# Kernel optimization log

Measured on AMD Instinct MI355X. Metric: run time of the kernel, lower is better.

## Reference

```python
import jax, jax.numpy as jnp
import numpy as np

B, H, L, D = 4, 4096, 8, 64  # queries shape [B, L, H, D]
FACTOR = 5
U = FACTOR * int(np.ceil(np.log(4096)))  # u_part = u = 45 (L_q == L_k)


def setup_inputs() -> dict:
    key = jax.random.key(0)
    kq, kk, kv, ki = jax.random.split(key, 4)
    queries = jax.random.normal(kq, (4, 4096, 8, 64), dtype=jnp.float32)
    keys = jax.random.normal(kk, (4, 4096, 8, 64), dtype=jnp.float32)
    values = jax.random.normal(kv, (4, 4096, 8, 64), dtype=jnp.float32)
    index_sample = jax.random.randint(ki, (4096, U), 0, 4096)  # torch.randint(key_length,(L_Q,sample_k))
    return {"queries": queries, "keys": keys, "values": values, "index_sample": index_sample}


def reference(queries, keys, values, index_sample):
    # (B, L, H, D) -> (B, H, L, D)
    q = jnp.transpose(queries, (0, 2, 1, 3))
    k = jnp.transpose(keys, (0, 2, 1, 3))
    v = jnp.transpose(values, (0, 2, 1, 3))
    b, h, l_q, d = q.shape
    l_k = k.shape[2]
    n_top = index_sample.shape[1]  # u == u_part == 45 here

    # --- _prob_QK: sampled QK scores (avoid materializing key_expand [B,H,Lq,Lk,D]) ---
    # key_sample: [B, H, Lq, sample_k, D]
    key_sample = k[:, :, index_sample, :]
    # Q_i . K_sampled: [B, H, Lq, sample_k]
    qk_sample = jnp.einsum('bhld,bhlsd->bhls', q, key_sample)
    # sparsity measure M = max - mean(over full key_length)
    m = jnp.max(qk_sample, axis=-1) - jnp.sum(qk_sample, axis=-1) / l_k  # [B,H,Lq]
    _, m_top = jax.lax.top_k(m, n_top)  # [B, H, u]

    # reduced queries: [B, H, u, D]
    q_reduce = jnp.take_along_axis(q, m_top[..., None], axis=2)
    scores_top = jnp.einsum('bhud,bhkd->bhuk', q_reduce, k)  # [B, H, u, Lk]

    scale = 1.0 / jnp.sqrt(jnp.asarray(d, dtype=q.dtype))
    scores_top = scores_top * scale

    # --- _get_initial_context (mask_flag=False): mean of values broadcast over queries ---
    context = jnp.broadcast_to(jnp.mean(v, axis=2, keepdims=True), (b, h, l_q, d))

    # --- _update_context: softmax + scatter attn@V into the top-u query rows ---
    attn = jax.nn.softmax(scores_top, axis=-1)  # [B, H, u, Lk]
    update = jnp.einsum('bhuk,bhkd->bhud', attn, v)  # [B, H, u, D]
    b_idx = jnp.arange(b)[:, None, None]
    h_idx = jnp.arange(h)[None, :, None]
    context = context.at[b_idx, h_idx, m_top].set(update)
    return context  # [B, H, Lq, D]
```

## Files before the change

kernel.cpp:

```cpp
#include <hip/hip_runtime.h>
#include <hip/hip_bf16.h>


#define NB 4
#define NH 8
#define NL 4096
#define ND 64
#define NS 45
#define SCALE 0.125f
#define NCHUNK 16
#define CHUNK 256

typedef float floatx4 __attribute__((ext_vector_type(4)));

static __device__ __forceinline__ float neg_inf() { return -__builtin_inff(); }

template <int CTRL>
static __device__ __forceinline__ float dpp_add(float x) {
  int y = __builtin_amdgcn_update_dpp(0, __builtin_bit_cast(int, x), CTRL,
                                      0xF, 0xF, true);
  return x + __builtin_bit_cast(float, y);
}
static __device__ __forceinline__ float red16(float x) {
  x = dpp_add<0x140>(x);
  x = dpp_add<0x141>(x);
  x = dpp_add<0x4E>(x);
  x = dpp_add<0xB1>(x);
  return x;
}
static __device__ __forceinline__ float red4(float x) {
  x = dpp_add<0xB1>(x);
  x = dpp_add<0x4E>(x);
  return x;
}

__global__ __launch_bounds__(256) void k_compute_m(
    const float* __restrict__ q, const float* __restrict__ k,
    const int* __restrict__ idxs, float* __restrict__ m_out)
{
  __shared__ int sidx[4][48];
  int gb = blockIdx.x;
  int pair = gb & 7;
  int b = pair >> 1, hg = pair & 1;
  int lg = gb >> 3;
  int t = threadIdx.x, w = t >> 6, lane = t & 63, g = lane >> 4;
  int l = lg * 4 + w;

  if (lane < NS) sidx[w][lane] = idxs[l * NS + lane];

  const floatx4* q4 =
      (const floatx4*)(q + ((size_t)(b * NL + l) * NH + hg * 4) * ND);
  floatx4 qr = __builtin_nontemporal_load(q4 + lane);

  const float* kbase = k + ((size_t)b * NL * NH + hg * 4) * ND;

  float mx = neg_inf(), sm = 0.f;
#pragma unroll 1
  for (int s0 = 0; s0 < NS; s0 += 9) {
    floatx4 kr[9];
#pragma unroll
    for (int j = 0; j < 9; j++) {
      int ki = __builtin_amdgcn_readfirstlane(sidx[w][s0 + j]);
      kr[j] = *((const floatx4*)(kbase + (size_t)ki * 512) + lane);
    }
    float p[9];
#pragma unroll
    for (int j = 0; j < 9; j++) {
      float d = kr[j].x * qr.x + kr[j].y * qr.y + kr[j].z * qr.z + kr[j].w * qr.w;
      p[j] = red16(d);
    }
    float m0 = fmaxf(fmaxf(p[0], p[1]), p[2]);
    float m1 = fmaxf(fmaxf(p[3], p[4]), p[5]);
    float m2 = fmaxf(fmaxf(p[6], p[7]), p[8]);
    mx = fmaxf(fmaxf(mx, m0), fmaxf(m1, m2));
    sm += ((p[0] + p[1]) + (p[2] + p[3])) +
          ((p[4] + p[5]) + (p[6] + p[7])) + p[8];
  }
  if ((lane & 15) == 0)
    m_out[((size_t)b * NH + hg * 4 + g) * NL + l] = mx - sm * (1.0f / 4096.0f);
}

__global__ __launch_bounds__(256) void k_topk_p1(
    const float* __restrict__ m_in, unsigned long long* __restrict__ cand)
{
  __shared__ unsigned long long keys[512];
  __shared__ unsigned long long wred[4];
  int blk = blockIdx.x;
  int bh = blk >> 3, slice = blk & 7;
  int t = threadIdx.x, wid = t >> 6, lane = t & 63;
  int base = slice * 512;
  for (int i = t; i < 512; i += 256) {
    float v = m_in[bh * NL + base + i];
    unsigned u = __float_as_uint(v);
    u ^= (u >> 31) ? 0xFFFFFFFFu : 0x80000000u;
    keys[i] = ((unsigned long long)u << 32) | (unsigned)(~(unsigned)(base + i));
  }
  __syncthreads();
  for (int it = 0; it < NS; ++it) {
    unsigned long long k0 = keys[t], k1 = keys[t + 256];
    unsigned long long best = k0 > k1 ? k0 : k1;
#pragma unroll
    for (int off = 32; off; off >>= 1) {
      unsigned long long o = __shfl_xor(best, off);
      if (o > best) best = o;
    }
    if (lane == 0) wred[wid] = best;
    __syncthreads();
    if (t == 0) {
      unsigned long long b0 = wred[0];
      if (wred[1] > b0) b0 = wred[1];
      if (wred[2] > b0) b0 = wred[2];
      if (wred[3] > b0) b0 = wred[3];
      cand[blk * NS + it] = b0;
      int gi = (int)(~(unsigned)(b0 & 0xFFFFFFFFull));
      keys[gi - base] = 0;
    }
    __syncthreads();
  }
}

__global__ __launch_bounds__(256) void k_topk_p2(
    const unsigned long long* __restrict__ cand, int* __restrict__ mtop)
{
  __shared__ unsigned long long keys[8 * NS];
  __shared__ unsigned long long wred[4];
  __shared__ unsigned long long sbest;
  int bh = blockIdx.x;
  int t = threadIdx.x, wid = t >> 6, lane = t & 63;
  for (int i = t; i < 8 * NS; i += 256) keys[i] = cand[bh * 8 * NS + i];
  __syncthreads();
  for (int it = 0; it < NS; ++it) {
    unsigned long long best = (t < 8 * NS) ? keys[t] : 0ull;
    if (t + 256 < 8 * NS) {
      unsigned long long k1 = keys[t + 256];
      if (k1 > best) best = k1;
    }
#pragma unroll
    for (int off = 32; off; off >>= 1) {
      unsigned long long o = __shfl_xor(best, off);
      if (o > best) best = o;
    }
    if (lane == 0) wred[wid] = best;
    __syncthreads();
    if (t == 0) {
      unsigned long long b0 = wred[0];
      if (wred[1] > b0) b0 = wred[1];
      if (wred[2] > b0) b0 = wred[2];
      if (wred[3] > b0) b0 = wred[3];
      sbest = b0;
      mtop[bh * NS + it] = (int)(~(unsigned)(b0 & 0xFFFFFFFFull));
    }
    __syncthreads();
    unsigned long long bb = sbest;
    if (t < 8 * NS && keys[t] == bb) keys[t] = 0;
    if (t + 256 < 8 * NS && keys[t + 256] == bb) keys[t + 256] = 0;
    __syncthreads();
  }
}

__global__ __launch_bounds__(256) void k_meanv_part(
    const float* __restrict__ v, float* __restrict__ vpart)
{
  __shared__ float part[4][ND];
  int bh = blockIdx.x, c = blockIdx.y;
  int b = bh >> 3, h = bh & 7;
  int t = threadIdx.x, d = t & 63, g = t >> 6;
  float a0 = 0.f, a1 = 0.f, a2 = 0.f, a3 = 0.f;
  const float* vb = v + ((size_t)(b * NL + c * 64) * NH + h) * ND + d;
#pragma unroll
  for (int i = 0; i < 4; i++) {
    a0 += vb[(size_t)(g + 4 * (4 * i + 0)) * NH * ND];
    a1 += vb[(size_t)(g + 4 * (4 * i + 1)) * NH * ND];
    a2 += vb[(size_t)(g + 4 * (4 * i + 2)) * NH * ND];
    a3 += vb[(size_t)(g + 4 * (4 * i + 3)) * NH * ND];
  }
  part[g][d] = (a0 + a1) + (a2 + a3);
  __syncthreads();
  if (g == 0) {
    float s = part[0][d] + part[1][d] + part[2][d] + part[3][d];
    vpart[(bh * 64 + c) * ND + d] = s;
  }
}

__global__ __launch_bounds__(64) void k_meanv_final(
    const float* __restrict__ vpart, float* __restrict__ meanv)
{
  int bh = blockIdx.x, d = threadIdx.x;
  float s = 0.f;
  for (int c = 0; c < 64; c++) s += vpart[(bh * 64 + c) * ND + d];
  meanv[bh * ND + d] = s * (1.0f / 4096.0f);
}

__global__ __launch_bounds__(256) void k_fill(
    const float* __restrict__ meanv, float4* __restrict__ out4)
{
  const int total = NB * NH * NL * ND / 4;
  const float4* mv4 = (const float4*)meanv;
  for (int i = blockIdx.x * 256 + threadIdx.x; i < total; i += gridDim.x * 256) {
    int bh = i >> 16;
    int d4 = i & 15;
    out4[i] = mv4[bh * 16 + d4];
  }
}

__global__ __launch_bounds__(1024) void k_scores(
    const float* __restrict__ q, const float* __restrict__ k,
    const float* __restrict__ v, const int* __restrict__ mtop,
    float* __restrict__ mc_out, float* __restrict__ lc_out,
    float* __restrict__ op_out)
{
  __shared__ float QLDS[NS * ND];
  __shared__ float SLDS[NS * 260];
  __shared__ int mt[NS];
  __shared__ float mcs[NS], lcs[NS];

  int gb = blockIdx.x;
  int xcd = gb & 7, seq = gb >> 3;
  int bh = xcd * 4 + (seq >> 4);
  int c = seq & 15;
  int b = bh >> 3, h = bh & 7;
  int t = threadIdx.x;
  int wid = t >> 6, lane = t & 63;

  if (t < NS) mt[t] = mtop[bh * NS + t];
  __syncthreads();

  const float4* q4 = (const float4*)q;
  float4* QL4 = (float4*)QLDS;
  if (t < NS * 16) {
    int u = t >> 4, j = t & 15;
    QL4[t] = q4[((size_t)(b * NL + mt[u]) * NH + h) * 16 + j];
  }
  __syncthreads();

  {
    int kk = wid * 16 + (lane >> 2);
    int seg = lane & 3;
    const float4* k4 =
        (const float4*)(k + ((size_t)(b * NL + c * CHUNK + kk) * NH + h) * ND)
        + seg * 4;
    float4 k0 = k4[0], k1 = k4[1], k2 = k4[2], k3 = k4[3];
    const float4* qp = QL4 + seg * 4;
    for (int u = 0; u < NS; ++u) {
      float4 a0 = qp[u * 16 + 0], a1 = qp[u * 16 + 1];
      float4 a2 = qp[u * 16 + 2], a3 = qp[u * 16 + 3];
      float dot = a0.x * k0.x + a0.y * k0.y + a0.z * k0.z + a0.w * k0.w
                + a1.x * k1.x + a1.y * k1.y + a1.z * k1.z + a1.w * k1.w
                + a2.x * k2.x + a2.y * k2.y + a2.z * k2.z + a2.w * k2.w
                + a3.x * k3.x + a3.y * k3.y + a3.z * k3.z + a3.w * k3.w;
      dot = red4(dot);
      if (seg == 0) SLDS[u * 260 + kk] = dot * SCALE;
    }
  }
  __syncthreads();

  for (int u = wid; u < NS; u += 16) {
    float4 sv = *(const float4*)&SLDS[u * 260 + lane * 4];
    float mx = fmaxf(fmaxf(sv.x, sv.y), fmaxf(sv.z, sv.w));
#pragma unroll
    for (int off = 32; off; off >>= 1) mx = fmaxf(mx, __shfl_xor(mx, off));
    float e0 = expf(sv.x - mx), e1 = expf(sv.y - mx);
    float e2 = expf(sv.z - mx), e3 = expf(sv.w - mx);
    float s = e0 + e1 + e2 + e3;
#pragma unroll
    for (int off = 32; off; off >>= 1) s += __shfl_xor(s, off);
    *(float4*)&SLDS[u * 260 + lane * 4] = make_float4(e0, e1, e2, e3);
    if (lane == 0) { mcs[u] = mx; lcs[u] = s; }
  }
  __syncthreads();

  float acc[3];
#pragma unroll
  for (int i = 0; i < 3; i++) acc[i] = 0.f;
  const float* vbase = v + ((size_t)(b * NL + c * CHUNK) * NH + h) * ND + lane;
  for (int kb = 0; kb < 64; ++kb) {
    float vd0 = vbase[(size_t)(kb * 4 + 0) * NH * ND];
    float vd1 = vbase[(size_t)(kb * 4 + 1) * NH * ND];
    float vd2 = vbase[(size_t)(kb * 4 + 2) * NH * ND];
    float vd3 = vbase[(size_t)(kb * 4 + 3) * NH * ND];
#pragma unroll
    for (int i = 0; i < 3; i++) {
      int u = wid + 16 * i;
      if (u < NS) {
        float4 p4 = *(const float4*)&SLDS[u * 260 + kb * 4];
        acc[i] += p4.x * vd0 + p4.y * vd1 + p4.z * vd2 + p4.w * vd3;
      }
    }
  }
#pragma unroll
  for (int i = 0; i < 3; i++) {
    int u = wid + 16 * i;
    if (u < NS)
      op_out[(((size_t)bh * NCHUNK + c) * NS + u) * ND + lane] = acc[i];
  }
  if (t < NS) {
    mc_out[(bh * NCHUNK + c) * NS + t] = mcs[t];
    lc_out[(bh * NCHUNK + c) * NS + t] = lcs[t];
  }
}

__global__ __launch_bounds__(256) void k_combine(
    const float* __restrict__ mc, const float* __restrict__ lc,
    const float* __restrict__ op, const int* __restrict__ mtop,
    float* __restrict__ out)
{
  int gw = blockIdx.x * 4 + (threadIdx.x >> 6);
  int lane = threadIdx.x & 63;
  int bh = gw / NS, u = gw % NS;
  float M = neg_inf();
  for (int c = 0; c < NCHUNK; c++)
    M = fmaxf(M, mc[(bh * NCHUNK + c) * NS + u]);
  float Lsum = 0.f, O = 0.f;
  for (int c = 0; c < NCHUNK; c++) {
    float e = expf(mc[(bh * NCHUNK + c) * NS + u] - M);
    Lsum += lc[(bh * NCHUNK + c) * NS + u] * e;
    O += op[(((size_t)bh * NCHUNK + c) * NS + u) * ND + lane] * e;
  }
  int row = mtop[bh * NS + u];
  out[((size_t)bh * NL + row) * ND + lane] = O / Lsum;
}

extern "C" void kernel_launch(void* const* d_in, const int* in_sizes, int n_in,
                              void* d_out, int out_size, void* d_ws, size_t ws_size,
                              hipStream_t stream) {
  const float* q = (const float*)d_in[0];
  const float* k = (const float*)d_in[1];
  const float* v = (const float*)d_in[2];
  const int* idxs = (const int*)d_in[3];
  float* out = (float*)d_out;
  float* ws = (float*)d_ws;

  float* m_ws  = ws;
  int*   mtop  = (int*)(ws + 131072);
  float* meanv = ws + 132512;
  float* mc    = ws + 134560;
  float* lc    = ws + 157600;
  float* op    = ws + 180640;
  float* vpart = op;
  unsigned long long* cand = (unsigned long long*)(op + 131072);

  hipLaunchKernelGGL(k_compute_m,   dim3(8192),      dim3(256),  0, stream, q, k, idxs, m_ws);
  hipLaunchKernelGGL(k_topk_p1,     dim3(256),       dim3(256),  0, stream, m_ws, cand);
  hipLaunchKernelGGL(k_topk_p2,     dim3(32),        dim3(256),  0, stream, cand, mtop);
  hipLaunchKernelGGL(k_meanv_part,  dim3(32, 64),    dim3(256),  0, stream, v, vpart);
  hipLaunchKernelGGL(k_meanv_final, dim3(32),        dim3(64),   0, stream, vpart, meanv);
  hipLaunchKernelGGL(k_fill,        dim3(2048),      dim3(256),  0, stream, meanv, (float4*)out);
  hipLaunchKernelGGL(k_scores,      dim3(512),       dim3(1024), 0, stream, q, k, v, mtop, mc, lc, op);
  hipLaunchKernelGGL(k_combine,     dim3(360),       dim3(256),  0, stream, mc, lc, op, mtop, out);
}
```

Before: 186.3 us.

## Fuse meanv, topk2 and fill into neighbouring kernels to cut launches

Merges the V partial-mean reduction into the sampled-QK kernel as extra blocks, and the final mean into the second top-k pass as extra blocks. The output fill becomes extra blocks of the scores kernel. The QK sampling now splits the 45 samples across two waves per query, with an LDS combine. The goal is to cut launch gaps and overlap independent memory-bound work, at the cost of heterogeneous blocks and a 1024-thread fill that may compete with scores for CUs.

```diff
diff --git a/kernel.cpp b/kernel.cpp
--- a/kernel.cpp
+++ b/kernel.cpp
@@ -34,50 +34,93 @@
   return x;
 }
 
-__global__ __launch_bounds__(256) void k_compute_m(
+template <int BS>
+static __device__ __forceinline__ void batch_dot(
+    const float* __restrict__ kbase, const int* __restrict__ srow, int s0,
+    floatx4 qr, int lane, float& mx, float& sm) {
+  floatx4 kr[BS];
+#pragma unroll
+  for (int j = 0; j < BS; j++) {
+    int ki = __builtin_amdgcn_readfirstlane(srow[s0 + j]);
+    kr[j] = *((const floatx4*)(kbase + (size_t)ki * 512) + lane);
+  }
+  float p[BS];
+#pragma unroll
+  for (int j = 0; j < BS; j++) {
+    float d = kr[j].x * qr.x + kr[j].y * qr.y + kr[j].z * qr.z + kr[j].w * qr.w;
+    p[j] = red16(d);
+  }
+#pragma unroll
+  for (int j = 0; j < BS; j++) { mx = fmaxf(mx, p[j]); sm += p[j]; }
+}
+
+__global__ __launch_bounds__(512) void kA_m_meanv(
     const float* __restrict__ q, const float* __restrict__ k,
-    const int* __restrict__ idxs, float* __restrict__ m_out)
+    const float* __restrict__ v, const int* __restrict__ idxs,
+    float* __restrict__ m_out, float* __restrict__ vpart)
 {
   __shared__ int sidx[4][48];
+  __shared__ float lmx[8][4], lsm[8][4];
+  __shared__ float part[8][ND];
   int gb = blockIdx.x;
-  int pair = gb & 7;
-  int b = pair >> 1, hg = pair & 1;
-  int lg = gb >> 3;
   int t = threadIdx.x, w = t >> 6, lane = t & 63, g = lane >> 4;
-  int l = lg * 4 + w;
-
-  if (lane < NS) sidx[w][lane] = idxs[l * NS + lane];
-
-  const floatx4* q4 =
-      (const floatx4*)(q + ((size_t)(b * NL + l) * NH + hg * 4) * ND);
-  floatx4 qr = __builtin_nontemporal_load(q4 + lane);
-
-  const float* kbase = k + ((size_t)b * NL * NH + hg * 4) * ND;
-
-  float mx = neg_inf(), sm = 0.f;
-#pragma unroll 1
-  for (int s0 = 0; s0 < NS; s0 += 9) {
-    floatx4 kr[9];
-#pragma unroll
-    for (int j = 0; j < 9; j++) {
-      int ki = __builtin_amdgcn_readfirstlane(sidx[w][s0 + j]);
-      kr[j] = *((const floatx4*)(kbase + (size_t)ki * 512) + lane);
-    }
-    float p[9];
-#pragma unroll
-    for (int j = 0; j < 9; j++) {
-      float d = kr[j].x * qr.x + kr[j].y * qr.y + kr[j].z * qr.z + kr[j].w * qr.w;
-      p[j] = red16(d);
-    }
-    float m0 = fmaxf(fmaxf(p[0], p[1]), p[2]);
-    float m1 = fmaxf(fmaxf(p[3], p[4]), p[5]);
-    float m2 = fmaxf(fmaxf(p[6], p[7]), p[8]);
-    mx = fmaxf(fmaxf(mx, m0), fmaxf(m1, m2));
-    sm += ((p[0] + p[1]) + (p[2] + p[3])) +
-          ((p[4] + p[5]) + (p[6] + p[7])) + p[8];
-  }
-  if ((lane & 15) == 0)
-    m_out[((size_t)b * NH + hg * 4 + g) * NL + l] = mx - sm * (1.0f / 4096.0f);
+
+  if (gb < 8192) {
+    int pair = gb & 7;
+    int b = pair >> 1, hg = pair & 1;
+    int lg = gb >> 3;
+    int wl = w & 3;
+    int l = lg * 4 + wl;
+
+    if (w < 4 && lane < NS) sidx[w][lane] = idxs[l * NS + lane];
+
+    const floatx4* q4 =
+        (const floatx4*)(q + ((size_t)(b * NL + l) * NH + hg * 4) * ND);
+    floatx4 qr = __builtin_nontemporal_load(q4 + lane);
+    const float* kbase = k + ((size_t)b * NL * NH + hg * 4) * ND;
+    const int* srow = sidx[wl];
+    __syncthreads();
+
+    float mx = neg_inf(), sm = 0.f;
+    if (w < 4) {
+      batch_dot<8>(kbase, srow, 0, qr, lane, mx, sm);
+      batch_dot<8>(kbase, srow, 8, qr, lane, mx, sm);
+      batch_dot<8>(kbase, srow, 16, qr, lane, mx, sm);
+    } else {
+      batch_dot<7>(kbase, srow, 24, qr, lane, mx, sm);
+      batch_dot<7>(kbase, srow, 31, qr, lane, mx, sm);
+      batch_dot<7>(kbase, srow, 38, qr, lane, mx, sm);
+    }
+    if ((lane & 15) == 0) { lmx[w][g] = mx; lsm[w][g] = sm; }
+    __syncthreads();
+    if (w < 4 && (lane & 15) == 0) {
+      float MX = fmaxf(lmx[w][g], lmx[w + 4][g]);
+      float SM = lsm[w][g] + lsm[w + 4][g];
+      m_out[((size_t)b * NH + hg * 4 + g) * NL + l] = MX - SM * (1.0f / 4096.0f);
+    }
+  } else {
+    int idx = gb - 8192;
+    int bh = idx >> 5, cc = idx & 31;
+    int b = bh >> 3, h = bh & 7;
+    int d = t & 63, gg = t >> 6;
+    float a0 = 0.f, a1 = 0.f, a2 = 0.f, a3 = 0.f;
+    const float* vb = v + ((size_t)(b * NL + cc * 128) * NH + h) * ND + d;
+#pragma unroll
+    for (int i = 0; i < 4; i++) {
+      a0 += vb[(size_t)(gg + 8 * (4 * i + 0)) * NH * ND];
+      a1 += vb[(size_t)(gg + 8 * (4 * i + 1)) * NH * ND];
+      a2 += vb[(size_t)(gg + 8 * (4 * i + 2)) * NH * ND];
+      a3 += vb[(size_t)(gg + 8 * (4 * i + 3)) * NH * ND];
+    }
+    part[gg][d] = (a0 + a1) + (a2 + a3);
+    __syncthreads();
+    if (gg == 0) {
+      float s = 0.f;
+#pragma unroll
+      for (int j = 0; j < 8; j++) s += part[j][d];
+      vpart[(bh * 32 + cc) * ND + d] = s;
+    }
+  }
 }
 
 __global__ __launch_bounds__(256) void k_topk_p1(
@@ -119,95 +162,69 @@
   }
 }
 
-__global__ __launch_bounds__(256) void k_topk_p2(
-    const unsigned long long* __restrict__ cand, int* __restrict__ mtop)
+__global__ __launch_bounds__(256) void kC_topk2_meanv(
+    const unsigned long long* __restrict__ cand, int* __restrict__ mtop,
+    const float* __restrict__ vpart, float* __restrict__ meanv)
 {
   __shared__ unsigned long long keys[8 * NS];
   __shared__ unsigned long long wred[4];
   __shared__ unsigned long long sbest;
-  int bh = blockIdx.x;
+  __shared__ float part2[4][ND];
+  int gb = blockIdx.x;
   int t = threadIdx.x, wid = t >> 6, lane = t & 63;
-  for (int i = t; i < 8 * NS; i += 256) keys[i] = cand[bh * 8 * NS + i];
-  __syncthreads();
-  for (int it = 0; it < NS; ++it) {
-    unsigned long long best = (t < 8 * NS) ? keys[t] : 0ull;
-    if (t + 256 < 8 * NS) {
-      unsigned long long k1 = keys[t + 256];
-      if (k1 > best) best = k1;
-    }
-#pragma unroll
-    for (int off = 32; off; off >>= 1) {
-      unsigned long long o = __shfl_xor(best, off);
-      if (o > best) best = o;
-    }
-    if (lane == 0) wred[wid] = best;
-    __syncthreads();
-    if (t == 0) {
-      unsigned long long b0 = wred[0];
-      if (wred[1] > b0) b0 = wred[1];
-      if (wred[2] > b0) b0 = wred[2];
-      if (wred[3] > b0) b0 = wred[3];
-      sbest = b0;
-      mtop[bh * NS + it] = (int)(~(unsigned)(b0 & 0xFFFFFFFFull));
-    }
-    __syncthreads();
-    unsigned long long bb = sbest;
-    if (t < 8 * NS && keys[t] == bb) keys[t] = 0;
-    if (t + 256 < 8 * NS && keys[t + 256] == bb) keys[t + 256] = 0;
-    __syncthreads();
-  }
-}
-
-__global__ __launch_bounds__(256) void k_meanv_part(
-    const float* __restrict__ v, float* __restrict__ vpart)
-{
-  __shared__ float part[4][ND];
-  int bh = blockIdx.x, c = blockIdx.y;
-  int b = bh >> 3, h = bh & 7;
-  int t = threadIdx.x, d = t & 63, g = t >> 6;
-  float a0 = 0.f, a1 = 0.f, a2 = 0.f, a3 = 0.f;
-  const float* vb = v + ((size_t)(b * NL + c * 64) * NH + h) * ND + d;
-#pragma unroll
-  for (int i = 0; i < 4; i++) {
-    a0 += vb[(size_t)(g + 4 * (4 * i + 0)) * NH * ND];
-    a1 += vb[(size_t)(g + 4 * (4 * i + 1)) * NH * ND];
-    a2 += vb[(size_t)(g + 4 * (4 * i + 2)) * NH * ND];
-    a3 += vb[(size_t)(g + 4 * (4 * i + 3)) * NH * ND];
-  }
-  part[g][d] = (a0 + a1) + (a2 + a3);
-  __syncthreads();
-  if (g == 0) {
-    float s = part[0][d] + part[1][d] + part[2][d] + part[3][d];
-    vpart[(bh * 64 + c) * ND + d] = s;
-  }
-}
-
-__global__ __launch_bounds__(64) void k_meanv_final(
-    const float* __restrict__ vpart, float* __restrict__ meanv)
-{
-  int bh = blockIdx.x, d = threadIdx.x;
-  float s = 0.f;
-  for (int c = 0; c < 64; c++) s += vpart[(bh * 64 + c) * ND + d];
-  meanv[bh * ND + d] = s * (1.0f / 4096.0f);
-}
-
-__global__ __launch_bounds__(256) void k_fill(
-    const float* __restrict__ meanv, float4* __restrict__ out4)
-{
-  const int total = NB * NH * NL * ND / 4;
-  const float4* mv4 = (const float4*)meanv;
-  for (int i = blockIdx.x * 256 + threadIdx.x; i < total; i += gridDim.x * 256) {
-    int bh = i >> 16;
-    int d4 = i & 15;
-    out4[i] = mv4[bh * 16 + d4];
-  }
-}
-
-__global__ __launch_bounds__(1024) void k_scores(
+
+  if (gb < 32) {
+    int bh = gb;
+    for (int i = t; i < 8 * NS; i += 256) keys[i] = cand[bh * 8 * NS + i];
+    __syncthreads();
+    for (int it = 0; it < NS; ++it) {
+      unsigned long long best = (t < 8 * NS) ? keys[t] : 0ull;
+      if (t + 256 < 8 * NS) {
+        unsigned long long k1 = keys[t + 256];
+        if (k1 > best) best = k1;
+      }
+#pragma unroll
+      for (int off = 32; off; off >>= 1) {
+        unsigned long long o = __shfl_xor(best, off);
+        if (o > best) best = o;
+      }
+      if (lane == 0) wred[wid] = best;
+      __syncthreads();
+      if (t == 0) {
+        unsigned long long b0 = wred[0];
+        if (wred[1] > b0) b0 = wred[1];
+        if (wred[2] > b0) b0 = wred[2];
+        if (wred[3] > b0) b0 = wred[3];
+        sbest = b0;
+        mtop[bh * NS + it] = (int)(~(unsigned)(b0 & 0xFFFFFFFFull));
+      }
+      __syncthreads();
+      unsigned long long bb = sbest;
+      if (t < 8 * NS && keys[t] == bb) keys[t] = 0;
+      if (t + 256 < 8 * NS && keys[t + 256] == bb) keys[t + 256] = 0;
+      __syncthreads();
+    }
+  } else {
+    int bh = gb - 32;
+    int d = t & 63, gg = t >> 6;
+    float s = 0.f;
+#pragma unroll
+    for (int i = 0; i < 8; i++) s += vpart[(bh * 32 + gg + 4 * i) * ND + d];
+    part2[gg][d] = s;
+    __syncthreads();
+    if (gg == 0) {
+      float tot = part2[0][d] + part2[1][d] + part2[2][d] + part2[3][d];
+      meanv[bh * ND + d] = tot * (1.0f / 4096.0f);
+    }
+  }
+}
+
+__global__ __launch_bounds__(1024) void kD_scores_fill(
     const float* __restrict__ q, const float* __restrict__ k,
     const float* __restrict__ v, const int* __restrict__ mtop,
+    const float* __restrict__ meanv,
     float* __restrict__ mc_out, float* __restrict__ lc_out,
-    float* __restrict__ op_out)
+    float* __restrict__ op_out, float4* __restrict__ out4)
 {
   __shared__ float QLDS[NS * ND];
   __shared__ float SLDS[NS * 260];
@@ -215,12 +232,23 @@
   __shared__ float mcs[NS], lcs[NS];
 
   int gb = blockIdx.x;
+  int t = threadIdx.x;
+  int wid = t >> 6, lane = t & 63;
+
+  if (gb >= 512) {
+    const int total = NB * NH * NL * ND / 4;
+    const float4* mv4 = (const float4*)meanv;
+    for (int i = (gb - 512) * 1024 + t; i < total; i += 512 * 1024) {
+      int bh = i >> 16;
+      out4[i] = mv4[bh * 16 + (i & 15)];
+    }
+    return;
+  }
+
   int xcd = gb & 7, seq = gb >> 3;
   int bh = xcd * 4 + (seq >> 4);
   int c = seq & 15;
   int b = bh >> 3, h = bh & 7;
-  int t = threadIdx.x;
-  int wid = t >> 6, lane = t & 63;
 
   if (t < NS) mt[t] = mtop[bh * NS + t];
   __syncthreads();
@@ -339,12 +367,14 @@
   float* vpart = op;
   unsigned long long* cand = (unsigned long long*)(op + 131072);
 
-  hipLaunchKernelGGL(k_compute_m,   dim3(8192),      dim3(256),  0, stream, q, k, idxs, m_ws);
-  hipLaunchKernelGGL(k_topk_p1,     dim3(256),       dim3(256),  0, stream, m_ws, cand);
-  hipLaunchKernelGGL(k_topk_p2,     dim3(32),        dim3(256),  0, stream, cand, mtop);
-  hipLaunchKernelGGL(k_meanv_part,  dim3(32, 64),    dim3(256),  0, stream, v, vpart);
-  hipLaunchKernelGGL(k_meanv_final, dim3(32),        dim3(64),   0, stream, vpart, meanv);
-  hipLaunchKernelGGL(k_fill,        dim3(2048),      dim3(256),  0, stream, meanv, (float4*)out);
-  hipLaunchKernelGGL(k_scores,      dim3(512),       dim3(1024), 0, stream, q, k, v, mtop, mc, lc, op);
-  hipLaunchKernelGGL(k_combine,     dim3(360),       dim3(256),  0, stream, mc, lc, op, mtop, out);
-}
+  hipLaunchKernelGGL(kA_m_meanv,     dim3(8192 + 1024), dim3(512),  0, stream,
+                     q, k, v, idxs, m_ws, vpart);
+  hipLaunchKernelGGL(k_topk_p1,      dim3(256),         dim3(256),  0, stream,
+                     m_ws, cand);
+  hipLaunchKernelGGL(kC_topk2_meanv, dim3(64),          dim3(256),  0, stream,
+                     cand, mtop, vpart, meanv);
+  hipLaunchKernelGGL(kD_scores_fill, dim3(1024),        dim3(1024), 0, stream,
+                     q, k, v, mtop, meanv, mc, lc, op, (float4*)out);
+  hipLaunchKernelGGL(k_combine,      dim3(360),         dim3(256),  0, stream,
+                     mc, lc, op, mtop, out);
+}
```

Measured after the change: 177.3 us. 1.05x faster.
